# Kernel tuning notes

Measured on AMD Instinct MI355X. Metric: run time of the kernel, lower is better.

Reference implementation:

```python
import jax, jax.numpy as jnp
import numpy as np

N_WIRES = 10
N_BLOCKS = 4
DIM = 2 ** N_WIRES


def _tables(n):
    # Basis-state bit tables. Wire 0 is the most-significant bit (torchquantum convention).
    s = np.arange(2 ** n)
    bits = (s[None, :] >> (n - 1 - np.arange(n))[:, None]) & 1  # [n, 2^n]
    zval = (1 - 2 * bits).astype(np.float32)  # PauliZ eigenvalue per wire per basis state
    # Composition of the circular CNOT ring (0,1),(1,2),...,(n-2,n-1),(n-1,0)
    # as a single basis permutation: state'[s] = state[P[s]].
    pairs = [(i, i + 1) for i in range(n - 1)] + [(n - 1, 0)]
    P = s.copy()
    for c, t in pairs:
        bit = (s >> (n - 1 - c)) & 1
        g = s ^ (bit << (n - 1 - t))  # CNOT maps new[s] = old[g(s)]
        P = P[g]
    return zval, P


_ZVAL_NP, _PERM_NP = _tables(N_WIRES)


def setup_inputs() -> dict:
    key = jax.random.key(0)
    k1, k2 = jax.random.split(key)
    x = jax.random.normal(k1, (2048, N_WIRES), jnp.float32)
    params = jax.random.normal(k2, (N_BLOCKS, 6, N_WIRES), jnp.float32)
    return {"x": x, "params": params}


def _rz_all(state, theta, zval):
    # RZ(theta_w) on every wire fused into one diagonal phase over the full statevector.
    # RZ = diag(e^{-i t/2}, e^{+i t/2}); exponent sign = -zval (bit0 -> -1).
    phase = jnp.exp((-0.5j) * (theta @ zval).astype(jnp.complex64))  # [2^n]
    return state * phase[None, :]


def _ry_all(state, theta, bsz):
    # RY(theta_w) on each wire w: 2x2 rotation applied along that wire's axis.
    for w in range(N_WIRES):
        left = 2 ** w
        right = DIM // (2 * left)
        s4 = state.reshape(bsz, left, 2, right)
        c = jnp.cos(theta[w] * 0.5)
        s_ = jnp.sin(theta[w] * 0.5)
        U = jnp.stack([jnp.stack([c, -s_]), jnp.stack([s_, c])]).astype(jnp.complex64)
        s4 = jnp.einsum('bixk,jx->bijk', s4, U)
        state = s4.reshape(bsz, DIM)
    return state


def reference(x, params):
    zval = jnp.asarray(_ZVAL_NP)
    perm = jnp.asarray(_PERM_NP)
    bsz = x.shape[0]
    state = jnp.zeros((bsz, DIM), jnp.complex64).at[:, 0].set(1.0)  # |0...0>
    for k in range(N_BLOCKS):
        p = params[k]
        # NOTE: the original module's "rx" layers are constructed with tq.RZ,
        # so each block is RZ, RY, RZ, CNOT-ring, RZ, RY, RZ, CNOT-ring.
        state = _rz_all(state, p[0], zval)
        state = _ry_all(state, p[1], bsz)
        state = _rz_all(state, p[2], zval)
        state = state[:, perm]
        state = _rz_all(state, p[3], zval)
        state = _ry_all(state, p[4], bsz)
        state = _rz_all(state, p[5], zval)
        state = state[:, perm]
        if k != N_BLOCKS - 1:
            # data re-uploading encoder: RZ(x[:, w]) on wire w, batch-dependent diagonal
            enc = jnp.exp((-0.5j) * (x @ zval).astype(jnp.complex64))  # [B, 2^n]
            state = state * enc
    probs = state.real ** 2 + state.imag ** 2  # [B, 2^n]
    out = probs @ zval.T  # MeasureAll PauliZ -> [B, n_wires]
    return out[None]  # [1, B, n_wires]
```

## Files before the change

### kernel.cpp

```cpp
#include <hip/hip_runtime.h>

#define NW 10

typedef float v2f __attribute__((ext_vector_type(2)));
typedef float v4f __attribute__((ext_vector_type(4)));

template<int CTRL>
__device__ __forceinline__ float fdpp(float v) {
    return __int_as_float(__builtin_amdgcn_mov_dpp(__float_as_int(v), CTRL, 0xF, 0xF, true));
}
template<int PAT>
__device__ __forceinline__ float fswz(float v) {
    return __int_as_float(__builtin_amdgcn_ds_swizzle(__float_as_int(v), PAT));
}

__device__ __forceinline__ int phi(int e) {
    return e ^ ((e & 0x10) >> 1) ^ ((e & 0x20) >> 4);
}

__global__ void precompute_kernel(const float* __restrict__ params, float4* __restrict__ tab4) {
    const int d = blockIdx.x;
    const int j = threadIdx.x;
    if (d < 7) {
        const int W = j >> 8, lane = j & 63, r = (j >> 6) & 3;
        const int s = (W << 8) | (lane << 2) | r;
        const int q = s ^ (s >> 1) ^ ((s & 1) * 0x300);
        const float* thA;
        const float* thB;
        if (d < 4) {
            thA = params + (d * 6 + 3) * NW;
            thB = params + (d * 6 + 2) * NW;
        } else {
            const int k = d - 4;
            thA = params + ((k + 1) * 6 + 0) * NW;
            thB = params + (k * 6 + 5) * NW;
        }
        float ang = 0.f;
#pragma unroll
        for (int w = 0; w < NW; ++w) {
            ang += thA[w] * (((s >> (9 - w)) & 1) ? 0.5f : -0.5f);
            ang += thB[w] * (((q >> (9 - w)) & 1) ? 0.5f : -0.5f);
        }
        float sn, cs;
        __sincosf(ang, &sn, &cs);
        tab4[d * 1024 + j] = make_float4(cs, sn, -sn, cs);
    } else if (j < 80) {
        const int ry = j / NW, w = j % NW;
        const int k = ry >> 1, i = ry & 1;
        const float* th = params + (k * 6 + (i ? 4 : 1)) * NW;
        float sn, cs;
        __sincosf(0.5f * th[w], &sn, &cs);
        float2* ryt = (float2*)(tab4 + 7 * 1024);
        ryt[j] = make_float2(cs, sn);
    }
}

__global__ __launch_bounds__(256, 4) void qsim_kernel(const float* __restrict__ x,
                                                      const v4f* __restrict__ tab4,
                                                      float* __restrict__ out) {
    __shared__ v2f buf[2][1024];
    __shared__ float sred[4][NW];

    const int t     = threadIdx.x;
    const int W     = t >> 6;
    const int lane  = t & 63;
    const int b     = blockIdx.x;
    const int ebase = lane | (W << 8);
    const float2* ry_tab = (const float2*)(tab4 + 7 * 1024);

    v2f st[4];
#pragma unroll
    for (int r = 0; r < 4; ++r) st[r] = (v2f){0.f, 0.f};
    if (t == 0) st[0].x = 1.f;

    const int wbase = phi(ebase);
    const int l0 = lane & 1, l1 = (lane >> 1) & 1, l2 = (lane >> 2) & 1,
              l3 = (lane >> 3) & 1, l4 = (lane >> 4) & 1, l5 = (lane >> 5) & 1;
    const int W0 = W & 1, W1 = (W >> 1) & 1;
    const int riA0 = l2 | (l4 << 1) | (l0 << 2) | (l5 << 3) | (l1 << 4) | (l3 << 5) | (W << 6);
    const int rgA  = phi(riA0);
    const int g0 = (l2 ^ l3) | ((l4 ^ l5) << 1) | ((l0 ^ l1) << 2) | ((l5 ^ W0) << 3)
                 | ((l1 ^ l2) << 4) | ((l3 ^ l4) << 5)
                 | ((W0 ^ W1) << 6) | (W1 << 7) | (l0 << 9);
    const int gP = phi(g0);

    const float* xb = x + b * NW;
    v2f xp[4];
    {
        float xv[NW];
#pragma unroll
        for (int w = 0; w < NW; ++w) xv[w] = xb[w];
        float A = 0.f;
#pragma unroll
        for (int w = 0; w < NW; ++w) A += xv[w];
        float hi = -0.5f * A;
        if (W & 2) hi += xv[0];
        if (W & 1) hi += xv[1];
#pragma unroll
        for (int j = 0; j < 6; ++j)
            hi += ((lane >> j) & 1) ? xv[7 - j] : 0.f;
        float lo[4];
        lo[0] = 0.f;   lo[1] = xv[9];
        lo[2] = xv[8]; lo[3] = xv[8] + xv[9];
#pragma unroll
        for (int r = 0; r < 4; ++r) {
            float sn, cs;
            __sincosf(hi + lo[r], &sn, &cs);
            xp[r] = (v2f){cs, sn};
        }
    }

    int bs = 0;
    v4f tq[4];

    auto pre = [&](int d) {
        const v4f* tb = tab4 + (d << 10) + ebase;
#pragma unroll
        for (int r = 0; r < 4; ++r) tq[r] = tb[r << 6];
    };
    auto apply_t = [&]() {
#pragma unroll
        for (int r = 0; r < 4; ++r)
            st[r] = st[r].x * tq[r].xy + st[r].y * tq[r].zw;
    };
    auto apply_tx = [&]() {
#pragma unroll
        for (int r = 0; r < 4; ++r) {
            const v2f c = xp[r].x * tq[r].xy + xp[r].y * tq[r].zw;
            const v2f cq = (v2f){-c.y, c.x};
            st[r] = st[r].x * c + st[r].y * cq;
        }
    };

    auto bfly_local = [&](float2 cw, int m) {
#pragma unroll
        for (int r = 0; r < 4; ++r) {
            if (!(r & m)) {
                const int r2 = r | m;
                const v2f a = st[r];
                st[r]  = cw.x * a - cw.y * st[r2];
                st[r2] = cw.y * a + cw.x * st[r2];
            }
        }
    };

    auto ry = [&](int ridx) {
        const float2* rt = ry_tab + ridx * NW;
        bfly_local(rt[9], 1);
        bfly_local(rt[8], 2);
        {   const float2 cw = rt[7]; const float ss = (lane & 1) ? cw.y : -cw.y;
#pragma unroll
            for (int r = 0; r < 4; ++r) {
                v2f p; p.x = fdpp<0xB1>(st[r].x); p.y = fdpp<0xB1>(st[r].y);
                st[r] = cw.x * st[r] + ss * p;
            }
        }
        {   const float2 cw = rt[6]; const float ss = (lane & 2) ? cw.y : -cw.y;
#pragma unroll
            for (int r = 0; r < 4; ++r) {
                v2f p; p.x = fdpp<0x4E>(st[r].x); p.y = fdpp<0x4E>(st[r].y);
                st[r] = cw.x * st[r] + ss * p;
            }
        }
        {   const float2 cw = rt[4]; const float ss = (lane & 8) ? cw.y : -cw.y;
#pragma unroll
            for (int r = 0; r < 4; ++r) {
                v2f p; p.x = fdpp<0x128>(st[r].x); p.y = fdpp<0x128>(st[r].y);
                st[r] = cw.x * st[r] + ss * p;
            }
        }
        {
            v2f* B = buf[bs]; bs ^= 1;
#pragma unroll
            for (int r = 0; r < 4; ++r)
                B[wbase + (r << 6)] = st[r];
            __syncthreads();
#pragma unroll
            for (int r = 0; r < 4; ++r)
                st[r] = B[rgA + (r << 8)];
        }
        bfly_local(rt[1], 1);
        bfly_local(rt[0], 2);
        {   const float2 cw = rt[5]; const float ss = (lane & 1) ? cw.y : -cw.y;
#pragma unroll
            for (int r = 0; r < 4; ++r) {
                v2f p; p.x = fdpp<0xB1>(st[r].x); p.y = fdpp<0xB1>(st[r].y);
                st[r] = cw.x * st[r] + ss * p;
            }
        }
        {   const float2 cw = rt[3]; const float ss = (lane & 2) ? cw.y : -cw.y;
#pragma unroll
            for (int r = 0; r < 4; ++r) {
                v2f p; p.x = fdpp<0x4E>(st[r].x); p.y = fdpp<0x4E>(st[r].y);
                st[r] = cw.x * st[r] + ss * p;
            }
        }
        {   const float2 cw = rt[2]; const float ss = (lane & 8) ? cw.y : -cw.y;
#pragma unroll
            for (int r = 0; r < 4; ++r) {
                v2f p; p.x = fdpp<0x128>(st[r].x); p.y = fdpp<0x128>(st[r].y);
                st[r] = cw.x * st[r] + ss * p;
            }
        }
    };

    auto perm = [&]() {
        v2f* B = buf[bs]; bs ^= 1;
#pragma unroll
        for (int r = 0; r < 4; ++r)
            B[wbase + (r << 6)] = st[r];
        __syncthreads();
        constexpr int xc[4] = {0, 0x1C0, 0x300, 0x2C0};
#pragma unroll
        for (int r = 0; r < 4; ++r)
            st[r] = B[gP ^ xc[r]];
    };

#pragma unroll 1
    for (int k = 0; k < 4; ++k) {
        pre(k);
        ry(2 * k);
        perm();
        apply_t();
        if (k < 3) pre(4 + k);
        ry(2 * k + 1);
        perm();
        if (k < 3) apply_tx();
    }

    float pr[4];
#pragma unroll
    for (int r = 0; r < 4; ++r) pr[r] = st[r].x * st[r].x + st[r].y * st[r].y;
    float S = 0.f;
#pragma unroll
    for (int r = 0; r < 4; ++r) S += pr[r];

    float acc[NW];
    acc[0] = (W & 2) ? -S : S;
    acc[1] = (W & 1) ? -S : S;
#pragma unroll
    for (int w = 2; w <= 7; ++w) {
        const int j = 7 - w;
        acc[w] = ((lane >> j) & 1) ? -S : S;
    }
    {
        float t8 = 0.f, t9 = 0.f;
#pragma unroll
        for (int r = 0; r < 4; ++r) {
            t8 += (r & 2) ? -pr[r] : pr[r];
            t9 += (r & 1) ? -pr[r] : pr[r];
        }
        acc[8] = t8; acc[9] = t9;
    }
#pragma unroll
    for (int w = 0; w < NW; ++w) {
        float a = acc[w];
        a += fdpp<0xB1>(a);
        a += fdpp<0x4E>(a);
        a += fswz<0x101F>(a);
        a += fdpp<0x128>(a);
        a += fswz<0x401F>(a);
        a += __shfl_xor(a, 32, 64);
        acc[w] = a;
    }
    if (lane == 0) {
#pragma unroll
        for (int w = 0; w < NW; ++w) sred[W][w] = acc[w];
    }
    __syncthreads();
    if (t < NW) out[b * NW + t] = sred[0][t] + sred[1][t] + sred[2][t] + sred[3][t];
}

extern "C" void kernel_launch(void* const* d_in, const int* in_sizes, int n_in,
                              void* d_out, int out_size, void* d_ws, size_t ws_size,
                              hipStream_t stream) {
    const float* x      = (const float*)d_in[0];
    const float* params = (const float*)d_in[1];
    float* out          = (float*)d_out;
    float4* tab4        = (float4*)d_ws;
    (void)in_sizes; (void)n_in; (void)out_size; (void)ws_size;
    precompute_kernel<<<8, 1024, 0, stream>>>(params, tab4);
    qsim_kernel<<<2048, 256, 0, stream>>>(x, (const v4f*)tab4, out);
}
```

Baseline: 80.13 us.

## Initialize first RY layer analytically and fold final CNOT permutation into measurement

The state starts at |0…0>, and the leading RZ only adds a global phase, so the first RY layer's output is a real product state. It is now computed in closed form per element instead of running the full butterfly network. The last permutation (shared-memory write, barrier, gather) is dropped, and the PauliZ signs for the final CNOT ring are folded into per-wire parity expressions at the measurement. This removes one full RY layer and one LDS shuffle with its barrier, at the cost of hand-derived bit-mapping logic that must exactly match the thread layout.

```diff
diff --git a/kernel.cpp b/kernel.cpp
--- a/kernel.cpp
+++ b/kernel.cpp
@@ -69,9 +69,6 @@
     const float2* ry_tab = (const float2*)(tab4 + 7 * 1024);
 
     v2f st[4];
-#pragma unroll
-    for (int r = 0; r < 4; ++r) st[r] = (v2f){0.f, 0.f};
-    if (t == 0) st[0].x = 1.f;
 
     const int wbase = phi(ebase);
     const int l0 = lane & 1, l1 = (lane >> 1) & 1, l2 = (lane >> 2) & 1,
@@ -132,6 +129,23 @@
         }
     };
 
+    auto init_L1 = [&]() {
+        const float2* rt = ry_tab;
+        float hi = (l0 ? rt[5].y : rt[5].x);
+        hi *= (l1 ? rt[3].y : rt[3].x);
+        hi *= (l2 ? rt[7].y : rt[7].x);
+        hi *= (l3 ? rt[2].y : rt[2].x);
+        hi *= (l4 ? rt[6].y : rt[6].x);
+        hi *= (l5 ? rt[4].y : rt[4].x);
+        hi *= (W0 ? rt[9].y : rt[9].x);
+        hi *= (W1 ? rt[8].y : rt[8].x);
+        const float c1 = rt[1].x, s1 = rt[1].y, c0 = rt[0].x, s0_ = rt[0].y;
+        st[0] = (v2f){hi * c1 * c0, 0.f};
+        st[1] = (v2f){hi * s1 * c0, 0.f};
+        st[2] = (v2f){hi * c1 * s0_, 0.f};
+        st[3] = (v2f){hi * s1 * s0_, 0.f};
+    };
+
     auto bfly_local = [&](float2 cw, int m) {
 #pragma unroll
         for (int r = 0; r < 4; ++r) {
@@ -219,39 +233,44 @@
 #pragma unroll 1
     for (int k = 0; k < 4; ++k) {
         pre(k);
-        ry(2 * k);
+        if (k == 0) init_L1();
+        else        ry(2 * k);
         perm();
         apply_t();
         if (k < 3) pre(4 + k);
         ry(2 * k + 1);
-        perm();
-        if (k < 3) apply_tx();
+        if (k < 3) {
+            perm();
+            apply_tx();
+        }
     }
 
     float pr[4];
 #pragma unroll
     for (int r = 0; r < 4; ++r) pr[r] = st[r].x * st[r].x + st[r].y * st[r].y;
-    float S = 0.f;
-#pragma unroll
-    for (int r = 0; r < 4; ++r) S += pr[r];
+    const float D = pr[0] - pr[1] - pr[2] + pr[3];
+    const float E = pr[0] - pr[1] + pr[2] - pr[3];
+    const int g2 = l3;
+    const int g3 = g2 ^ l1;
+    const int g4 = g3 ^ l5;
+    const int g5 = g4 ^ l0;
+    const int g6 = g5 ^ l4;
+    const int g7 = g6 ^ l2;
+    const int g8 = g7 ^ W1;
+    const int g9 = g8 ^ W0;
 
     float acc[NW];
-    acc[0] = (W & 2) ? -S : S;
-    acc[1] = (W & 1) ? -S : S;
-#pragma unroll
-    for (int w = 2; w <= 7; ++w) {
-        const int j = 7 - w;
-        acc[w] = ((lane >> j) & 1) ? -S : S;
-    }
-    {
-        float t8 = 0.f, t9 = 0.f;
-#pragma unroll
-        for (int r = 0; r < 4; ++r) {
-            t8 += (r & 2) ? -pr[r] : pr[r];
-            t9 += (r & 1) ? -pr[r] : pr[r];
-        }
-        acc[8] = t8; acc[9] = t9;
-    }
+    acc[0] = g9 ? -E : E;
+    acc[1] = D;
+    acc[2] = g2 ? -D : D;
+    acc[3] = g3 ? -D : D;
+    acc[4] = g4 ? -D : D;
+    acc[5] = g5 ? -D : D;
+    acc[6] = g6 ? -D : D;
+    acc[7] = g7 ? -D : D;
+    acc[8] = g8 ? -D : D;
+    acc[9] = g9 ? -D : D;
+
 #pragma unroll
     for (int w = 0; w < NW; ++w) {
         float a = acc[w];
```

New measurement: 79.93 us. No clear change (-0.2%).
